# Optimization experiments

Measured on AMD Instinct MI355X. Metric: run time of the kernel, lower is better.

Reference implementation:

```python
import jax, jax.numpy as jnp
import numpy as np

B, S, DIM, HEADS, DH = 1, 192, 512, 8, 64
LN_EPS = 1e-5


def setup_inputs() -> dict:
    key = jax.random.key(0)
    ks = jax.random.split(key, 5)
    rn = lambda k, shp: jax.random.normal(k, shp, dtype=jnp.float32) * 0.02
    return {
        "x": jax.random.normal(ks[0], (B, S, DIM), dtype=jnp.float32),
        "ln_w": jnp.ones((DIM,), jnp.float32),
        "ln_b": jnp.zeros((DIM,), jnp.float32),
        "W_abcde": rn(ks[1], (5 * HEADS * DH, DIM)),
        "b_abcde": jnp.zeros((5 * HEADS * DH,), jnp.float32),
        "W_K": rn(ks[2], (HEADS, DH, DH, DH)),
        "W_V": rn(ks[3], (HEADS, DH, DH, DH)),
        "W_out": rn(ks[4], (DIM, HEADS * DH)),
        "b_out": jnp.zeros((DIM,), jnp.float32),
    }


def reference(x, ln_w, ln_b, W_abcde, b_abcde, W_K, W_V, W_out, b_out):
    b, n, _ = x.shape
    # LayerNorm (biased variance, eps=1e-5, affine)
    mu = jnp.mean(x, axis=-1, keepdims=True)
    var = jnp.var(x, axis=-1, keepdims=True)
    xn = (x - mu) / jnp.sqrt(var + LN_EPS) * ln_w + ln_b
    # abcde projection, chunk into 5, split heads -> [b, n, h, d]
    proj = xn @ W_abcde.T + b_abcde
    a_, b_, c_, d_, e_ = [t.reshape(b, n, HEADS, DH) for t in jnp.split(proj, 5, axis=-1)]
    # cubic attention score chain (note: heads summed out in step2, reintroduced by a_)
    step1 = jnp.einsum('brnk,nijk->brij', c_, W_K)          # [b, r, d, d]
    step2 = jnp.einsum('brij,bqnj->briq', step1, b_)        # [b, r, d, q] (sum over heads of b_)
    attn = jnp.einsum('briq,bpni->bnpqr', step2, a_)        # [b, h, p, q, r]
    # "causal" mask: positions where p >= q set to 1e-6 (faithful to masked_fill_)
    t_idx = jnp.arange(n)[:, None, None]
    s_idx = jnp.arange(n)[None, :, None]
    mask = (t_idx >= s_idx)[None, None]                      # [1,1,p,q,1]
    attn = jnp.where(mask, jnp.float32(1e-6), attn)
    # 'b n p1 p2 p3 -> b n p3 (p1 p2)', scale by 1/dim_head, softmax over (p1 p2)
    attn = attn.transpose(0, 1, 4, 2, 3).reshape(b, HEADS, n, n * n) / DH
    attn = jax.nn.softmax(attn, axis=-1)
    # pairwise values: [b, p1, p2, h, d] -> 'b p s n h -> b n h (p s)'
    v = jnp.einsum('bpnh,bqng,nhgf->bpqnf', d_, e_, W_V)
    v = v.transpose(0, 3, 4, 1, 2).reshape(b, HEADS, DH, n * n)
    # weighted sum over pair axis, merge heads
    z = jnp.einsum('bnql,bnhl->bqnh', attn, v).reshape(b, n, HEADS * DH)
    return z @ W_out.T + b_out
```

## Files before the change

### kernel.cpp

```cpp
#include <hip/hip_runtime.h>
#include <hip/hip_bf16.h>
#include <cstdint>

#define SEQ 192

typedef float f32x4 __attribute__((ext_vector_type(4)));
typedef float f32x8 __attribute__((ext_vector_type(8)));
typedef __bf16 bf16;
typedef __bf16 bf16x8 __attribute__((ext_vector_type(8)));
typedef __bf16 bf16x4 __attribute__((ext_vector_type(4)));

#define MFMA_BF16(a, b, c) __builtin_amdgcn_mfma_f32_16x16x32_bf16(a, b, c, 0, 0, 0)

__device__ __forceinline__ bf16x8 cvt8(f32x8 v) {
  bf16x8 o;
#pragma unroll
  for (int i = 0; i < 8; i++) o[i] = (bf16)v[i];
  return o;
}

__global__ __launch_bounds__(256) void k1_prep(
    const float* __restrict__ x, const float* __restrict__ ln_w, const float* __restrict__ ln_b,
    const float* __restrict__ WV, bf16* __restrict__ xn_bf, bf16* __restrict__ WVt2) {
  int bid = blockIdx.x, tid = threadIdx.x;
  if (bid < 512) {
    int g = bid & 63, hh = bid >> 6;
    __shared__ float ld[64 * 65];
    int f = tid & 63, r4 = tid >> 6;
#pragma unroll
    for (int it = 0; it < 16; it++) {
      int hp = it * 4 + r4;
      ld[hp * 65 + f] = WV[(((size_t)(hh * 64 + hp) * 64 + g) * 64) + f];
    }
    __syncthreads();
    int hp2 = tid & 63;
#pragma unroll
    for (int it = 0; it < 16; it++) {
      int ff = it * 4 + r4;
      WVt2[(size_t)hh * 262144 + (size_t)(ff * 64 + g) * 64 + hp2] = (bf16)ld[hp2 * 65 + ff];
    }
    return;
  }
  bid -= 512;
  {
    int r = bid;
    const float* xr = x + (size_t)r * 512;
    float v0 = xr[tid], v1 = xr[tid + 256];
    float s = v0 + v1, s2 = v0 * v0 + v1 * v1;
#pragma unroll
    for (int off = 32; off > 0; off >>= 1) {
      s += __shfl_down(s, off);
      s2 += __shfl_down(s2, off);
    }
    __shared__ float redS[4], redS2[4];
    int wave = tid >> 6, lane = tid & 63;
    if (lane == 0) { redS[wave] = s; redS2[wave] = s2; }
    __syncthreads();
    float S = redS[0] + redS[1] + redS[2] + redS[3];
    float S2 = redS2[0] + redS2[1] + redS2[2] + redS2[3];
    float mean = S * (1.0f / 512.0f);
    float var = S2 * (1.0f / 512.0f) - mean * mean;
    float rstd = rsqrtf(var + 1e-5f);
    bf16* xnr = xn_bf + (size_t)r * 512;
    xnr[tid] = (bf16)((v0 - mean) * rstd * ln_w[tid] + ln_b[tid]);
    xnr[tid + 256] = (bf16)((v1 - mean) * rstd * ln_w[tid + 256] + ln_b[tid + 256]);
  }
}

template <int MODE>
__device__ __forceinline__ void gemm_body(const bf16* __restrict__ A, const bf16* __restrict__ Bt,
                                          bf16* __restrict__ C1, int N, int K,
                                          int nb, int mb, int tid) {
  int n0 = nb * 64, m0 = mb * 64;
  int wave = tid >> 6, lane = tid & 63;
  int lq = lane >> 4, l16 = lane & 15;
  const bf16* Ap = A + (size_t)(m0 + wave * 16 + l16) * K;
  f32x4 acc[4];
#pragma unroll
  for (int nt = 0; nt < 4; nt++) acc[nt] = (f32x4){0.f, 0.f, 0.f, 0.f};
  for (int k0 = 0; k0 < K; k0 += 32) {
    bf16x8 af = *(const bf16x8*)(Ap + k0 + lq * 8);
#pragma unroll
    for (int nt = 0; nt < 4; nt++) {
      bf16x8 bv = *(const bf16x8*)(Bt + (size_t)(n0 + nt * 16 + l16) * K + k0 + lq * 8);
      acc[nt] = MFMA_BF16(af, bv, acc[nt]);
    }
  }
  int cm = m0 + wave * 16 + lq * 4;
#pragma unroll
  for (int nt = 0; nt < 4; nt++) {
    int n = n0 + nt * 16 + l16;
    if constexpr (MODE == 1) {
#pragma unroll
      for (int rg = 0; rg < 4; rg++) C1[(size_t)(cm + rg) * N + n] = (bf16)acc[nt][rg];
    } else {
      int r = cm >> 6, i0 = cm & 63;
      bf16x4 pk = {(bf16)acc[nt][0], (bf16)acc[nt][1], (bf16)acc[nt][2], (bf16)acc[nt][3]};
      *(bf16x4*)(C1 + (size_t)r * 12288 + (size_t)n * 64 + i0) = pk;
    }
  }
}

__global__ __launch_bounds__(256) void k2_proj(
    const bf16* __restrict__ xn_bf, const float* __restrict__ Wab,
    const float* __restrict__ b_abcde, float* __restrict__ proj, bf16* __restrict__ a_bf,
    bf16* __restrict__ c_bf, bf16* __restrict__ d_bf) {
  int bid = blockIdx.x, tid = threadIdx.x;
  int nb = bid % 40, mb = bid / 40;
  int n0 = nb * 64, m0 = mb * 64;
  int wave = tid >> 6, lane = tid & 63;
  int lq = lane >> 4, l16 = lane & 15;
  const bf16* Ap = xn_bf + (size_t)(m0 + wave * 16 + l16) * 512;
  f32x4 acc[4];
#pragma unroll
  for (int nt = 0; nt < 4; nt++) acc[nt] = (f32x4){0.f, 0.f, 0.f, 0.f};
  for (int k0 = 0; k0 < 512; k0 += 32) {
    bf16x8 af = *(const bf16x8*)(Ap + k0 + lq * 8);
#pragma unroll
    for (int nt = 0; nt < 4; nt++) {
      f32x8 wv = *(const f32x8*)(Wab + (size_t)(n0 + nt * 16 + l16) * 512 + k0 + lq * 8);
      acc[nt] = MFMA_BF16(af, cvt8(wv), acc[nt]);
    }
  }
  int cm = m0 + wave * 16 + lq * 4;
#pragma unroll
  for (int nt = 0; nt < 4; nt++) {
    int n = n0 + nt * 16 + l16;
    int chunk = n >> 9, hcol = (n >> 6) & 7, i = n & 63;
#pragma unroll
    for (int rg = 0; rg < 4; rg++) {
      int m = cm + rg;
      float v = acc[nt][rg] + b_abcde[n];
      proj[(size_t)m * 2560 + n] = v;
      bf16 bv = (bf16)v;
      if (chunk == 0) a_bf[((size_t)hcol * SEQ + m) * 64 + i] = bv;
      else if (chunk == 2) c_bf[(size_t)m * 512 + (n - 1024)] = bv;
      else if (chunk == 3) d_bf[((size_t)hcol * SEQ + m) * 64 + i] = bv;
    }
  }
}

__global__ __launch_bounds__(256) void k3_mid(
    const bf16* __restrict__ c_bf, const float* __restrict__ WK, bf16* __restrict__ s1bf,
    const bf16* __restrict__ d_bf, const bf16* __restrict__ WVt2, bf16* __restrict__ tTt,
    const float* __restrict__ proj, bf16* __restrict__ eT_bf, float* __restrict__ ecum,
    bf16* __restrict__ bsum_bf) {
  __shared__ float el[64 * 65];
  int bid = blockIdx.x, tid = threadIdx.x;
  if (bid < 192) {
    int nb = bid % 64, mb = bid / 64;
    int n0 = nb * 64, m0 = mb * 64;
    int wave = tid >> 6, lane = tid & 63;
    int lq = lane >> 4, l16 = lane & 15;
    const bf16* Ap = c_bf + (size_t)(m0 + wave * 16 + l16) * 512;
    f32x4 acc[4];
#pragma unroll
    for (int nt = 0; nt < 4; nt++) acc[nt] = (f32x4){0.f, 0.f, 0.f, 0.f};
    size_t offn[4];
#pragma unroll
    for (int nt = 0; nt < 4; nt++) {
      int n = n0 + nt * 16 + l16;
      offn[nt] = (size_t)(n >> 6) * 4096 + (size_t)(n & 63) * 64;
    }
    for (int k0 = 0; k0 < 512; k0 += 32) {
      bf16x8 af = *(const bf16x8*)(Ap + k0 + lq * 8);
      size_t kb = (size_t)(k0 >> 6) * 262144 + (k0 & 32) + lq * 8;
#pragma unroll
      for (int nt = 0; nt < 4; nt++) {
        f32x8 wv = *(const f32x8*)(WK + kb + offn[nt]);
        acc[nt] = MFMA_BF16(af, cvt8(wv), acc[nt]);
      }
    }
    int cm = m0 + wave * 16 + lq * 4;
#pragma unroll
    for (int nt = 0; nt < 4; nt++) {
      int n = n0 + nt * 16 + l16;
#pragma unroll
      for (int rg = 0; rg < 4; rg++) s1bf[(size_t)(cm + rg) * 4096 + n] = (bf16)acc[nt][rg];
    }
    return;
  }
  bid -= 192;
  if (bid < 1536) {
    int h = bid / 192, rem = bid % 192;
    gemm_body<1>(d_bf + (size_t)h * 12288, WVt2 + (size_t)h * 262144,
                 tTt + (size_t)h * 786432, 4096, 64, rem % 64, rem / 64, tid);
    return;
  }
  bid -= 1536;
  if (bid < 8) {
    int h = bid;
    float carry = 0.f;
    for (int ch = 0; ch < 3; ch++) {
      int pbase = ch * 64;
      for (int idx = tid; idx < 4096; idx += 256) {
        int pl = idx >> 6, g = idx & 63;
        el[pl * 65 + g] = proj[(size_t)(pbase + pl) * 2560 + 2048 + h * 64 + g];
      }
      __syncthreads();
      for (int idx = tid; idx < 4096; idx += 256) {
        int g = idx >> 6, ql = idx & 63;
        eT_bf[((size_t)h * 64 + g) * SEQ + pbase + ql] = (bf16)el[ql * 65 + g];
      }
      if (tid < 64) {
        float run = carry;
        for (int pl = 0; pl < 64; pl++) {
          run += el[pl * 65 + tid];
          ecum[(size_t)h * 12288 + (pbase + pl) * 64 + tid] = run;
        }
        carry = run;
      }
      __syncthreads();
    }
    return;
  }
  bid -= 8;
  {
    int j = tid & 63, qg = tid >> 6;
#pragma unroll
    for (int qi = 0; qi < 16; qi++) {
      int q = bid * 64 + qg * 16 + qi;
      float s = 0.f;
#pragma unroll
      for (int hh = 0; hh < 8; hh++) s += proj[(size_t)q * 2560 + 512 + hh * 64 + j];
      bsum_bf[q * 64 + j] = (bf16)s;
    }
  }
}

__global__ __launch_bounds__(256) void k4_step2(const bf16* __restrict__ s1bf,
                                                const bf16* __restrict__ bsum_bf,
                                                bf16* __restrict__ s2bf) {
  int bid = blockIdx.x;
  gemm_body<2>(s1bf, bsum_bf, s2bf, 192, 64, bid % 3, bid / 3, threadIdx.x);
}

__global__ __launch_bounds__(256, 3) void k5_attn(
    const bf16* __restrict__ a_bf, const bf16* __restrict__ s2bf,
    const bf16* __restrict__ eT_bf, const float* __restrict__ ecum,
    bf16* __restrict__ ew_bf, float* __restrict__ Lsum) {
  int r = blockIdx.x, h = blockIdx.y;
  int tid = threadIdx.x, wave = tid >> 6, lane = tid & 63;
  int lq = lane >> 4, l16 = lane & 15;
  __shared__ __align__(16) bf16 wch[2][4][3][16 * 40];
  __shared__ float redL[4];
  int pt[3] = {wave, wave + 4, 11 - wave};

  const bf16* ah = a_bf + (size_t)h * 12288;
  const bf16* s2r = s2bf + (size_t)r * 12288;
  const bf16* eh = eT_bf + (size_t)h * 12288;
  const float* ech = ecum + (size_t)h * 12288;

  bf16x8 afr[3][2];
#pragma unroll
  for (int mt = 0; mt < 3; mt++)
#pragma unroll
    for (int kc = 0; kc < 2; kc++)
      afr[mt][kc] = *(const bf16x8*)(ah + (pt[mt] * 16 + l16) * 64 + kc * 32 + lq * 8);

  f32x4 ewacc[3][4];
#pragma unroll
  for (int mt = 0; mt < 3; mt++)
#pragma unroll
    for (int nt = 0; nt < 4; nt++) ewacc[mt][nt] = (f32x4){0.f, 0.f, 0.f, 0.f};
  float lpart = 0.f;

  for (int c = 0; c < 6; c++) {
    if (c * 32 + 31 <= wave * 16) continue;
    int par = c & 1;
    bf16x8 efr[4];
#pragma unroll
    for (int nt = 0; nt < 4; nt++)
      efr[nt] = *(const bf16x8*)(eh + (nt * 16 + l16) * SEQ + c * 32 + lq * 8);
    bf16x8 bq[2][2];
#pragma unroll
    for (int sub = 0; sub < 2; sub++) {
      int q = c * 32 + sub * 16 + l16;
      bq[sub][0] = *(const bf16x8*)(s2r + q * 64 + lq * 8);
      bq[sub][1] = *(const bf16x8*)(s2r + q * 64 + 32 + lq * 8);
    }
    f32x4 sacc[3][2];
#pragma unroll
    for (int mt = 0; mt < 3; mt++) {
      if (c * 32 + 31 <= pt[mt] * 16) continue;
#pragma unroll
      for (int sub = 0; sub < 2; sub++) {
        if (c * 32 + sub * 16 + 15 <= pt[mt] * 16) continue;
        f32x4 sv = (f32x4){0.f, 0.f, 0.f, 0.f};
        sv = MFMA_BF16(afr[mt][0], bq[sub][0], sv);
        sacc[mt][sub] = MFMA_BF16(afr[mt][1], bq[sub][1], sv);
      }
    }
#pragma unroll
    for (int mt = 0; mt < 3; mt++) {
      if (c * 32 + 31 <= pt[mt] * 16) continue;
      bf16* mybuf = &wch[par][wave][mt][0];
#pragma unroll
      for (int sub = 0; sub < 2; sub++) {
        if (c * 32 + sub * 16 + 15 <= pt[mt] * 16) {
#pragma unroll
          for (int rg = 0; rg < 4; rg++) mybuf[(lq * 4 + rg) * 40 + sub * 16 + l16] = (bf16)0.f;
          continue;
        }
        int q = c * 32 + sub * 16 + l16;
        int p0 = pt[mt] * 16 + lq * 4;
#pragma unroll
        for (int rg = 0; rg < 4; rg++) {
          float wv = (q > p0 + rg) ? __expf(sacc[mt][sub][rg] * 0.015625f) : 0.f;
          lpart += wv;
          mybuf[(lq * 4 + rg) * 40 + sub * 16 + l16] = (bf16)wv;
        }
      }
    }
#pragma unroll
    for (int mt = 0; mt < 3; mt++) {
      if (c * 32 + 31 <= pt[mt] * 16) continue;
      bf16x8 wf = *(const bf16x8*)(&wch[par][wave][mt][l16 * 40 + lq * 8]);
#pragma unroll
      for (int nt = 0; nt < 4; nt++) ewacc[mt][nt] = MFMA_BF16(wf, efr[nt], ewacc[mt][nt]);
    }
  }

  bf16* ewout = ew_bf + ((size_t)h * SEQ + r) * 12288;
#pragma unroll
  for (int mt = 0; mt < 3; mt++)
#pragma unroll
    for (int nt = 0; nt < 4; nt++)
#pragma unroll
      for (int rg = 0; rg < 4; rg++) {
        int p = pt[mt] * 16 + lq * 4 + rg;
        int g = nt * 16 + l16;
        ewout[p * 64 + g] = (bf16)(ewacc[mt][nt][rg] + ech[p * 64 + g]);
      }

#pragma unroll
  for (int off = 32; off > 0; off >>= 1) lpart += __shfl_down(lpart, off);
  if (lane == 0) redL[wave] = lpart;
  __syncthreads();
  if (tid == 0) Lsum[h * SEQ + r] = redL[0] + redL[1] + redL[2] + redL[3];
}

__global__ __launch_bounds__(512) void k5b_z(
    const bf16* __restrict__ ew_bf, const bf16* __restrict__ tTt, float* __restrict__ Zpart) {
  int h = blockIdx.x, mt = blockIdx.y, ks = blockIdx.z;
  int tid = threadIdx.x, wave = tid >> 6, lane = tid & 63;
  int lq = lane >> 4, l16 = lane & 15;
  __shared__ float zred[8][16][66];
  const bf16* ewh = ew_bf + ((size_t)h * SEQ + mt * 32) * 12288;
  const bf16* th = tTt + (size_t)h * 786432;
  f32x4 acc[2][4];
#pragma unroll
  for (int m2 = 0; m2 < 2; m2++)
#pragma unroll
    for (int nt = 0; nt < 4; nt++) acc[m2][nt] = (f32x4){0.f, 0.f, 0.f, 0.f};
  for (int jj = 0; jj < 6; jj++) {
    int kc = ks * 48 + wave * 6 + jj;
    int p = kc >> 1, g0 = (kc & 1) * 32;
    bf16x8 af0 = *(const bf16x8*)(ewh + (size_t)l16 * 12288 + kc * 32 + lq * 8);
    bf16x8 af1 = *(const bf16x8*)(ewh + (size_t)(16 + l16) * 12288 + kc * 32 + lq * 8);
#pragma unroll
    for (int nt = 0; nt < 4; nt++) {
      bf16x8 tf = *(const bf16x8*)(th + (size_t)p * 4096 + (nt * 16 + l16) * 64 + g0 + lq * 8);
      acc[0][nt] = MFMA_BF16(af0, tf, acc[0][nt]);
      acc[1][nt] = MFMA_BF16(af1, tf, acc[1][nt]);
    }
  }
#pragma unroll
  for (int m2 = 0; m2 < 2; m2++) {
    if (m2) __syncthreads();
#pragma unroll
    for (int nt = 0; nt < 4; nt++)
#pragma unroll
      for (int rg = 0; rg < 4; rg++) zred[wave][lq * 4 + rg][nt * 16 + l16] = acc[m2][nt][rg];
    __syncthreads();
#pragma unroll
    for (int o = 0; o < 2; o++) {
      int idx = o * 512 + tid;
      int rloc = idx >> 6, f = idx & 63;
      float s = 0.f;
#pragma unroll
      for (int wv = 0; wv < 8; wv++) s += zred[wv][rloc][f];
      Zpart[(size_t)ks * 98304 + (size_t)(mt * 32 + m2 * 16 + rloc) * 512 + h * 64 + f] = s;
    }
  }
}

__global__ __launch_bounds__(256) void k5c_zf(const float* __restrict__ Zpart,
                                              const float* __restrict__ Lsum,
                                              bf16* __restrict__ z_bf) {
  int m = blockIdx.x, tid = threadIdx.x;
#pragma unroll
  for (int o = 0; o < 2; o++) {
    int c = o * 256 + tid;
    int h = c >> 6;
    float s = 0.f;
#pragma unroll
    for (int ks = 0; ks < 8; ks++) s += Zpart[(size_t)ks * 98304 + (size_t)m * 512 + c];
    float L = Lsum[h * SEQ + m] + 18528.0f;
    z_bf[(size_t)m * 512 + c] = (bf16)(s / L);
  }
}

__global__ __launch_bounds__(256) void k6_out(
    const bf16* __restrict__ z_bf, const float* __restrict__ Wout,
    const float* __restrict__ b_out, float* __restrict__ out) {
  int bid = blockIdx.x, tid = threadIdx.x;
  int nb = bid & 7, mb = bid >> 3;
  int wave = tid >> 6, lane = tid & 63;
  int lq = lane >> 4, l16 = lane & 15;
  int m = mb * 16 + l16;
  f32x4 acc[4];
#pragma unroll
  for (int nt = 0; nt < 4; nt++) acc[nt] = (f32x4){0.f, 0.f, 0.f, 0.f};
#pragma unroll
  for (int kc = 0; kc < 4; kc++) {
    int k0 = wave * 128 + kc * 32;
    bf16x8 af = *(const bf16x8*)(z_bf + (size_t)m * 512 + k0 + lq * 8);
#pragma unroll
    for (int nt = 0; nt < 4; nt++) {
      f32x8 wv = *(const f32x8*)(Wout + (size_t)(nb * 64 + nt * 16 + l16) * 512 + k0 + lq * 8);
      acc[nt] = MFMA_BF16(af, cvt8(wv), acc[nt]);
    }
  }
  __shared__ float red[4][16][68];
#pragma unroll
  for (int nt = 0; nt < 4; nt++)
#pragma unroll
    for (int rg = 0; rg < 4; rg++) red[wave][lq * 4 + rg][nt * 16 + l16] = acc[nt][rg];
  __syncthreads();
#pragma unroll
  for (int o = 0; o < 4; o++) {
    int idx = o * 256 + tid;
    int rloc = idx >> 6, f = idx & 63;
    float s = red[0][rloc][f] + red[1][rloc][f] + red[2][rloc][f] + red[3][rloc][f];
    out[(size_t)(mb * 16 + rloc) * 512 + nb * 64 + f] = s + b_out[nb * 64 + f];
  }
}

static const size_t OFF_PROJ = 0;
static const size_t OFF_ECUM = 491520;
static const size_t OFF_XN = 589824;
static const size_t OFF_ZPART = 638976;
static const size_t OFF_LSUM = 1425408;
static const size_t OFF_Z = 1427456;
static const size_t OFF_WVT = 2473984;
static const size_t OFF_A = 3522560;
static const size_t OFF_C = 3571712;
static const size_t OFF_D = 3620864;
static const size_t OFF_ET = 3670016;
static const size_t OFF_BSUM = 3719168;
static const size_t OFF_S1 = 3725312;
static const size_t OFF_S2 = 4118528;
static const size_t OFF_TT = 5298176;
static const size_t OFF_EW = 8493056;

extern "C" void kernel_launch(void* const* d_in, const int* in_sizes, int n_in,
                              void* d_out, int out_size, void* d_ws, size_t ws_size,
                              hipStream_t stream) {
  (void)in_sizes; (void)n_in; (void)out_size; (void)ws_size;
  const float* x = (const float*)d_in[0];
  const float* ln_w = (const float*)d_in[1];
  const float* ln_b = (const float*)d_in[2];
  const float* W_abcde = (const float*)d_in[3];
  const float* b_abcde = (const float*)d_in[4];
  const float* W_K = (const float*)d_in[5];
  const float* W_V = (const float*)d_in[6];
  const float* W_out = (const float*)d_in[7];
  const float* b_out = (const float*)d_in[8];
  float* out = (float*)d_out;
  float* ws = (float*)d_ws;

  float* proj = ws + OFF_PROJ;
  float* ecum = ws + OFF_ECUM;
  bf16* xn_bf = (bf16*)(ws + OFF_XN);
  float* Zpart = ws + OFF_ZPART;
  float* Lsum = ws + OFF_LSUM;
  bf16* z_bf = (bf16*)(ws + OFF_Z);
  bf16* WVt2 = (bf16*)(ws + OFF_WVT);
  bf16* a_bf = (bf16*)(ws + OFF_A);
  bf16* c_bf = (bf16*)(ws + OFF_C);
  bf16* d_bf = (bf16*)(ws + OFF_D);
  bf16* eT_bf = (bf16*)(ws + OFF_ET);
  bf16* bsum_bf = (bf16*)(ws + OFF_BSUM);
  bf16* s1bf = (bf16*)(ws + OFF_S1);
  bf16* s2bf = (bf16*)(ws + OFF_S2);
  bf16* tTt = (bf16*)(ws + OFF_TT);
  bf16* ew_bf = (bf16*)(ws + OFF_EW);

  k1_prep<<<704, 256, 0, stream>>>(x, ln_w, ln_b, W_V, xn_bf, WVt2);
  k2_proj<<<120, 256, 0, stream>>>(xn_bf, W_abcde, b_abcde, proj, a_bf, c_bf, d_bf);
  k3_mid<<<1739, 256, 0, stream>>>(c_bf, W_K, s1bf, d_bf, WVt2, tTt, proj, eT_bf, ecum,
                                   bsum_bf);
  k4_step2<<<576, 256, 0, stream>>>(s1bf, bsum_bf, s2bf);
  k5_attn<<<dim3(SEQ, 8), 256, 0, stream>>>(a_bf, s2bf, eT_bf, ecum, ew_bf, Lsum);
  k5b_z<<<dim3(8, 6, 8), 512, 0, stream>>>(ew_bf, tTt, Zpart);
  k5c_zf<<<SEQ, 256, 0, stream>>>(Zpart, Lsum, z_bf);
  k6_out<<<96, 256, 0, stream>>>(z_bf, W_out, b_out, out);
}
```

Before: 214.9 us.

## Fuse pipeline into one cooperative persistent kernel with grid syncs

Measured after the change: 588.3 us. +173.8%, slower.

```diff
diff --git a/kernel.cpp b/kernel.cpp
--- a/kernel.cpp
+++ b/kernel.cpp
@@ -1,8 +1,12 @@
 #include <hip/hip_runtime.h>
+#include <hip/hip_cooperative_groups.h>
 #include <hip/hip_bf16.h>
 #include <cstdint>
 
+namespace cg = cooperative_groups;
+
 #define SEQ 192
+#define GRID 512
 
 typedef float f32x4 __attribute__((ext_vector_type(4)));
 typedef float f32x8 __attribute__((ext_vector_type(8)));
@@ -19,32 +23,67 @@
   return o;
 }
 
-__global__ __launch_bounds__(256) void k1_prep(
-    const float* __restrict__ x, const float* __restrict__ ln_w, const float* __restrict__ ln_b,
-    const float* __restrict__ WV, bf16* __restrict__ xn_bf, bf16* __restrict__ WVt2) {
-  int bid = blockIdx.x, tid = threadIdx.x;
-  if (bid < 512) {
-    int g = bid & 63, hh = bid >> 6;
-    __shared__ float ld[64 * 65];
+struct P {
+  const float *x, *ln_w, *ln_b, *Wab, *b_ab, *WK, *WV, *Wout, *b_out;
+  float *out, *proj, *ecum, *Zpart, *Lsum;
+  bf16 *xn, *WVt2, *a, *c, *d, *eT, *bsum, *s1, *s2, *tTt, *ew;
+};
+
+template <int MODE>
+__device__ __forceinline__ void gemm_body(const bf16* __restrict__ A, const bf16* __restrict__ Bt,
+                                          bf16* __restrict__ C1, int N, int K, int nb, int mb,
+                                          int tid) {
+  int n0 = nb * 64, m0 = mb * 64;
+  int wave = tid >> 6, lane = tid & 63;
+  int lq = lane >> 4, l16 = lane & 15;
+  const bf16* Ap = A + (size_t)(m0 + wave * 16 + l16) * K;
+  f32x4 acc[4];
+#pragma unroll
+  for (int nt = 0; nt < 4; nt++) acc[nt] = (f32x4){0.f, 0.f, 0.f, 0.f};
+  for (int k0 = 0; k0 < K; k0 += 32) {
+    bf16x8 af = *(const bf16x8*)(Ap + k0 + lq * 8);
+#pragma unroll
+    for (int nt = 0; nt < 4; nt++) {
+      bf16x8 bv = *(const bf16x8*)(Bt + (size_t)(n0 + nt * 16 + l16) * K + k0 + lq * 8);
+      acc[nt] = MFMA_BF16(af, bv, acc[nt]);
+    }
+  }
+  int cm = m0 + wave * 16 + lq * 4;
+#pragma unroll
+  for (int nt = 0; nt < 4; nt++) {
+    int n = n0 + nt * 16 + l16;
+    if constexpr (MODE == 1) {
+#pragma unroll
+      for (int rg = 0; rg < 4; rg++) C1[(size_t)(cm + rg) * N + n] = (bf16)acc[nt][rg];
+    } else {
+      int r = cm >> 6, i0 = cm & 63;
+      bf16x4 pk = {(bf16)acc[nt][0], (bf16)acc[nt][1], (bf16)acc[nt][2], (bf16)acc[nt][3]};
+      *(bf16x4*)(C1 + (size_t)r * 12288 + (size_t)n * 64 + i0) = pk;
+    }
+  }
+}
+
+__device__ __forceinline__ void ph1(const P& p, char* sm, int u, int tid) {
+  if (u < 512) {
+    int g = u & 63, hh = u >> 6;
+    float* ld = (float*)sm;
     int f = tid & 63, r4 = tid >> 6;
 #pragma unroll
     for (int it = 0; it < 16; it++) {
       int hp = it * 4 + r4;
-      ld[hp * 65 + f] = WV[(((size_t)(hh * 64 + hp) * 64 + g) * 64) + f];
+      ld[hp * 65 + f] = p.WV[(((size_t)(hh * 64 + hp) * 64 + g) * 64) + f];
     }
     __syncthreads();
     int hp2 = tid & 63;
 #pragma unroll
     for (int it = 0; it < 16; it++) {
       int ff = it * 4 + r4;
-      WVt2[(size_t)hh * 262144 + (size_t)(ff * 64 + g) * 64 + hp2] = (bf16)ld[hp2 * 65 + ff];
-    }
-    return;
-  }
-  bid -= 512;
-  {
-    int r = bid;
-    const float* xr = x + (size_t)r * 512;
+      p.WVt2[(size_t)hh * 262144 + (size_t)(ff * 64 + g) * 64 + hp2] = (bf16)ld[hp2 * 65 + ff];
+    }
+    __syncthreads();
+  } else {
+    int r = u - 512;
+    const float* xr = p.x + (size_t)r * 512;
     float v0 = xr[tid], v1 = xr[tid + 256];
     float s = v0 + v1, s2 = v0 * v0 + v1 * v1;
 #pragma unroll
@@ -52,7 +91,8 @@
       s += __shfl_down(s, off);
       s2 += __shfl_down(s2, off);
     }
-    __shared__ float redS[4], redS2[4];
+    float* redS = (float*)(sm + 16640);
+    float* redS2 = redS + 4;
     int wave = tid >> 6, lane = tid & 63;
     if (lane == 0) { redS[wave] = s; redS2[wave] = s2; }
     __syncthreads();
@@ -61,56 +101,19 @@
     float mean = S * (1.0f / 512.0f);
     float var = S2 * (1.0f / 512.0f) - mean * mean;
     float rstd = rsqrtf(var + 1e-5f);
-    bf16* xnr = xn_bf + (size_t)r * 512;
-    xnr[tid] = (bf16)((v0 - mean) * rstd * ln_w[tid] + ln_b[tid]);
-    xnr[tid + 256] = (bf16)((v1 - mean) * rstd * ln_w[tid + 256] + ln_b[tid + 256]);
-  }
-}
-
-template <int MODE>
-__device__ __forceinline__ void gemm_body(const bf16* __restrict__ A, const bf16* __restrict__ Bt,
-                                          bf16* __restrict__ C1, int N, int K,
-                                          int nb, int mb, int tid) {
+    bf16* xnr = p.xn + (size_t)r * 512;
+    xnr[tid] = (bf16)((v0 - mean) * rstd * p.ln_w[tid] + p.ln_b[tid]);
+    xnr[tid + 256] = (bf16)((v1 - mean) * rstd * p.ln_w[tid + 256] + p.ln_b[tid + 256]);
+    __syncthreads();
+  }
+}
+
+__device__ __forceinline__ void ph2(const P& p, int u, int tid) {
+  int nb = u % 40, mb = u / 40;
   int n0 = nb * 64, m0 = mb * 64;
   int wave = tid >> 6, lane = tid & 63;
   int lq = lane >> 4, l16 = lane & 15;
-  const bf16* Ap = A + (size_t)(m0 + wave * 16 + l16) * K;
-  f32x4 acc[4];
-#pragma unroll
-  for (int nt = 0; nt < 4; nt++) acc[nt] = (f32x4){0.f, 0.f, 0.f, 0.f};
-  for (int k0 = 0; k0 < K; k0 += 32) {
-    bf16x8 af = *(const bf16x8*)(Ap + k0 + lq * 8);
-#pragma unroll
-    for (int nt = 0; nt < 4; nt++) {
-      bf16x8 bv = *(const bf16x8*)(Bt + (size_t)(n0 + nt * 16 + l16) * K + k0 + lq * 8);
-      acc[nt] = MFMA_BF16(af, bv, acc[nt]);
-    }
-  }
-  int cm = m0 + wave * 16 + lq * 4;
-#pragma unroll
-  for (int nt = 0; nt < 4; nt++) {
-    int n = n0 + nt * 16 + l16;
-    if constexpr (MODE == 1) {
-#pragma unroll
-      for (int rg = 0; rg < 4; rg++) C1[(size_t)(cm + rg) * N + n] = (bf16)acc[nt][rg];
-    } else {
-      int r = cm >> 6, i0 = cm & 63;
-      bf16x4 pk = {(bf16)acc[nt][0], (bf16)acc[nt][1], (bf16)acc[nt][2], (bf16)acc[nt][3]};
-      *(bf16x4*)(C1 + (size_t)r * 12288 + (size_t)n * 64 + i0) = pk;
-    }
-  }
-}
-
-__global__ __launch_bounds__(256) void k2_proj(
-    const bf16* __restrict__ xn_bf, const float* __restrict__ Wab,
-    const float* __restrict__ b_abcde, float* __restrict__ proj, bf16* __restrict__ a_bf,
-    bf16* __restrict__ c_bf, bf16* __restrict__ d_bf) {
-  int bid = blockIdx.x, tid = threadIdx.x;
-  int nb = bid % 40, mb = bid / 40;
-  int n0 = nb * 64, m0 = mb * 64;
-  int wave = tid >> 6, lane = tid & 63;
-  int lq = lane >> 4, l16 = lane & 15;
-  const bf16* Ap = xn_bf + (size_t)(m0 + wave * 16 + l16) * 512;
+  const bf16* Ap = p.xn + (size_t)(m0 + wave * 16 + l16) * 512;
   f32x4 acc[4];
 #pragma unroll
   for (int nt = 0; nt < 4; nt++) acc[nt] = (f32x4){0.f, 0.f, 0.f, 0.f};
@@ -118,7 +121,7 @@
     bf16x8 af = *(const bf16x8*)(Ap + k0 + lq * 8);
 #pragma unroll
     for (int nt = 0; nt < 4; nt++) {
-      f32x8 wv = *(const f32x8*)(Wab + (size_t)(n0 + nt * 16 + l16) * 512 + k0 + lq * 8);
+      f32x8 wv = *(const f32x8*)(p.Wab + (size_t)(n0 + nt * 16 + l16) * 512 + k0 + lq * 8);
       acc[nt] = MFMA_BF16(af, cvt8(wv), acc[nt]);
     }
   }
@@ -130,126 +133,106 @@
 #pragma unroll
     for (int rg = 0; rg < 4; rg++) {
       int m = cm + rg;
-      float v = acc[nt][rg] + b_abcde[n];
-      proj[(size_t)m * 2560 + n] = v;
+      float v = acc[nt][rg] + p.b_ab[n];
+      p.proj[(size_t)m * 2560 + n] = v;
       bf16 bv = (bf16)v;
-      if (chunk == 0) a_bf[((size_t)hcol * SEQ + m) * 64 + i] = bv;
-      else if (chunk == 2) c_bf[(size_t)m * 512 + (n - 1024)] = bv;
-      else if (chunk == 3) d_bf[((size_t)hcol * SEQ + m) * 64 + i] = bv;
-    }
-  }
-}
-
-__global__ __launch_bounds__(256) void k3_mid(
-    const bf16* __restrict__ c_bf, const float* __restrict__ WK, bf16* __restrict__ s1bf,
-    const bf16* __restrict__ d_bf, const bf16* __restrict__ WVt2, bf16* __restrict__ tTt,
-    const float* __restrict__ proj, bf16* __restrict__ eT_bf, float* __restrict__ ecum,
-    bf16* __restrict__ bsum_bf) {
-  __shared__ float el[64 * 65];
-  int bid = blockIdx.x, tid = threadIdx.x;
-  if (bid < 192) {
-    int nb = bid % 64, mb = bid / 64;
-    int n0 = nb * 64, m0 = mb * 64;
-    int wave = tid >> 6, lane = tid & 63;
-    int lq = lane >> 4, l16 = lane & 15;
-    const bf16* Ap = c_bf + (size_t)(m0 + wave * 16 + l16) * 512;
-    f32x4 acc[4];
-#pragma unroll
-    for (int nt = 0; nt < 4; nt++) acc[nt] = (f32x4){0.f, 0.f, 0.f, 0.f};
-    size_t offn[4];
-#pragma unroll
-    for (int nt = 0; nt < 4; nt++) {
-      int n = n0 + nt * 16 + l16;
-      offn[nt] = (size_t)(n >> 6) * 4096 + (size_t)(n & 63) * 64;
-    }
-    for (int k0 = 0; k0 < 512; k0 += 32) {
-      bf16x8 af = *(const bf16x8*)(Ap + k0 + lq * 8);
-      size_t kb = (size_t)(k0 >> 6) * 262144 + (k0 & 32) + lq * 8;
-#pragma unroll
-      for (int nt = 0; nt < 4; nt++) {
-        f32x8 wv = *(const f32x8*)(WK + kb + offn[nt]);
-        acc[nt] = MFMA_BF16(af, cvt8(wv), acc[nt]);
-      }
-    }
-    int cm = m0 + wave * 16 + lq * 4;
-#pragma unroll
-    for (int nt = 0; nt < 4; nt++) {
-      int n = n0 + nt * 16 + l16;
-#pragma unroll
-      for (int rg = 0; rg < 4; rg++) s1bf[(size_t)(cm + rg) * 4096 + n] = (bf16)acc[nt][rg];
-    }
-    return;
-  }
-  bid -= 192;
-  if (bid < 1536) {
-    int h = bid / 192, rem = bid % 192;
-    gemm_body<1>(d_bf + (size_t)h * 12288, WVt2 + (size_t)h * 262144,
-                 tTt + (size_t)h * 786432, 4096, 64, rem % 64, rem / 64, tid);
-    return;
-  }
-  bid -= 1536;
-  if (bid < 8) {
-    int h = bid;
+      if (chunk == 0) p.a[((size_t)hcol * SEQ + m) * 64 + i] = bv;
+      else if (chunk == 2) p.c[(size_t)m * 512 + (n - 1024)] = bv;
+      else if (chunk == 3) p.d[((size_t)hcol * SEQ + m) * 64 + i] = bv;
+    }
+  }
+}
+
+__device__ __forceinline__ void ph3(const P& p, char* sm, int u, int tid) {
+  if (u < 8) {
+    int h = u;
+    float* el = (float*)sm;
     float carry = 0.f;
     for (int ch = 0; ch < 3; ch++) {
       int pbase = ch * 64;
+      if (ch) __syncthreads();
       for (int idx = tid; idx < 4096; idx += 256) {
         int pl = idx >> 6, g = idx & 63;
-        el[pl * 65 + g] = proj[(size_t)(pbase + pl) * 2560 + 2048 + h * 64 + g];
+        el[pl * 65 + g] = p.proj[(size_t)(pbase + pl) * 2560 + 2048 + h * 64 + g];
       }
       __syncthreads();
       for (int idx = tid; idx < 4096; idx += 256) {
         int g = idx >> 6, ql = idx & 63;
-        eT_bf[((size_t)h * 64 + g) * SEQ + pbase + ql] = (bf16)el[ql * 65 + g];
+        p.eT[((size_t)h * 64 + g) * SEQ + pbase + ql] = (bf16)el[ql * 65 + g];
       }
       if (tid < 64) {
         float run = carry;
         for (int pl = 0; pl < 64; pl++) {
           run += el[pl * 65 + tid];
-          ecum[(size_t)h * 12288 + (pbase + pl) * 64 + tid] = run;
+          p.ecum[(size_t)h * 12288 + (pbase + pl) * 64 + tid] = run;
         }
         carry = run;
       }
       __syncthreads();
     }
-    return;
-  }
-  bid -= 8;
-  {
+  } else if (u < 11) {
+    int b3 = u - 8;
     int j = tid & 63, qg = tid >> 6;
 #pragma unroll
     for (int qi = 0; qi < 16; qi++) {
-      int q = bid * 64 + qg * 16 + qi;
+      int q = b3 * 64 + qg * 16 + qi;
       float s = 0.f;
 #pragma unroll
-      for (int hh = 0; hh < 8; hh++) s += proj[(size_t)q * 2560 + 512 + hh * 64 + j];
-      bsum_bf[q * 64 + j] = (bf16)s;
-    }
-  }
-}
-
-__global__ __launch_bounds__(256) void k4_step2(const bf16* __restrict__ s1bf,
-                                                const bf16* __restrict__ bsum_bf,
-                                                bf16* __restrict__ s2bf) {
-  int bid = blockIdx.x;
-  gemm_body<2>(s1bf, bsum_bf, s2bf, 192, 64, bid % 3, bid / 3, threadIdx.x);
-}
-
-__global__ __launch_bounds__(256, 3) void k5_attn(
-    const bf16* __restrict__ a_bf, const bf16* __restrict__ s2bf,
-    const bf16* __restrict__ eT_bf, const float* __restrict__ ecum,
-    bf16* __restrict__ ew_bf, float* __restrict__ Lsum) {
-  int r = blockIdx.x, h = blockIdx.y;
-  int tid = threadIdx.x, wave = tid >> 6, lane = tid & 63;
+      for (int hh = 0; hh < 8; hh++) s += p.proj[(size_t)q * 2560 + 512 + hh * 64 + j];
+      p.bsum[q * 64 + j] = (bf16)s;
+    }
+  } else if (u < 203) {
+    int unit = u - 11;
+    int nb = unit & 63, mb = unit >> 6;
+    int n0 = nb * 64, m0 = mb * 64;
+    int wave = tid >> 6, lane = tid & 63;
+    int lq = lane >> 4, l16 = lane & 15;
+    const bf16* Ap = p.c + (size_t)(m0 + wave * 16 + l16) * 512;
+    f32x4 acc[4];
+#pragma unroll
+    for (int nt = 0; nt < 4; nt++) acc[nt] = (f32x4){0.f, 0.f, 0.f, 0.f};
+    size_t offn[4];
+#pragma unroll
+    for (int nt = 0; nt < 4; nt++) {
+      int n = n0 + nt * 16 + l16;
+      offn[nt] = (size_t)(n >> 6) * 4096 + (size_t)(n & 63) * 64;
+    }
+    for (int k0 = 0; k0 < 512; k0 += 32) {
+      bf16x8 af = *(const bf16x8*)(Ap + k0 + lq * 8);
+      size_t kb = (size_t)(k0 >> 6) * 262144 + (k0 & 32) + lq * 8;
+#pragma unroll
+      for (int nt = 0; nt < 4; nt++) {
+        f32x8 wv = *(const f32x8*)(p.WK + kb + offn[nt]);
+        acc[nt] = MFMA_BF16(af, cvt8(wv), acc[nt]);
+      }
+    }
+    int cm = m0 + wave * 16 + lq * 4;
+#pragma unroll
+    for (int nt = 0; nt < 4; nt++) {
+      int n = n0 + nt * 16 + l16;
+#pragma unroll
+      for (int rg = 0; rg < 4; rg++) p.s1[(size_t)(cm + rg) * 4096 + n] = (bf16)acc[nt][rg];
+    }
+  } else {
+    int unit = u - 203;
+    int h = unit / 192, rem = unit % 192;
+    gemm_body<1>(p.d + (size_t)h * 12288, p.WVt2 + (size_t)h * 262144,
+                 p.tTt + (size_t)h * 786432, 4096, 64, rem % 64, rem / 64, tid);
+  }
+}
+
+__device__ __forceinline__ void ph5(const P& p, char* sm, int u, int tid) {
+  int h = u & 7, r = u >> 3;
+  int wave = tid >> 6, lane = tid & 63;
   int lq = lane >> 4, l16 = lane & 15;
-  __shared__ __align__(16) bf16 wch[2][4][3][16 * 40];
-  __shared__ float redL[4];
+  bf16* wch = (bf16*)sm;
+  float* redL = (float*)(sm + 30720);
   int pt[3] = {wave, wave + 4, 11 - wave};
 
-  const bf16* ah = a_bf + (size_t)h * 12288;
-  const bf16* s2r = s2bf + (size_t)r * 12288;
-  const bf16* eh = eT_bf + (size_t)h * 12288;
-  const float* ech = ecum + (size_t)h * 12288;
+  const bf16* ah = p.a + (size_t)h * 12288;
+  const bf16* s2r = p.s2 + (size_t)r * 12288;
+  const bf16* eh = p.eT + (size_t)h * 12288;
+  const float* ech = p.ecum + (size_t)h * 12288;
 
   bf16x8 afr[3][2];
 #pragma unroll
@@ -265,27 +248,27 @@
     for (int nt = 0; nt < 4; nt++) ewacc[mt][nt] = (f32x4){0.f, 0.f, 0.f, 0.f};
   float lpart = 0.f;
 
-  for (int c = 0; c < 6; c++) {
-    if (c * 32 + 31 <= wave * 16) continue;
-    int par = c & 1;
+  for (int cc = 0; cc < 6; cc++) {
+    if (cc * 32 + 31 <= wave * 16) continue;
+    int par = cc & 1;
     bf16x8 efr[4];
 #pragma unroll
     for (int nt = 0; nt < 4; nt++)
-      efr[nt] = *(const bf16x8*)(eh + (nt * 16 + l16) * SEQ + c * 32 + lq * 8);
+      efr[nt] = *(const bf16x8*)(eh + (nt * 16 + l16) * SEQ + cc * 32 + lq * 8);
     bf16x8 bq[2][2];
 #pragma unroll
     for (int sub = 0; sub < 2; sub++) {
-      int q = c * 32 + sub * 16 + l16;
+      int q = cc * 32 + sub * 16 + l16;
       bq[sub][0] = *(const bf16x8*)(s2r + q * 64 + lq * 8);
       bq[sub][1] = *(const bf16x8*)(s2r + q * 64 + 32 + lq * 8);
     }
     f32x4 sacc[3][2];
 #pragma unroll
     for (int mt = 0; mt < 3; mt++) {
-      if (c * 32 + 31 <= pt[mt] * 16) continue;
+      if (cc * 32 + 31 <= pt[mt] * 16) continue;
 #pragma unroll
       for (int sub = 0; sub < 2; sub++) {
-        if (c * 32 + sub * 16 + 15 <= pt[mt] * 16) continue;
+        if (cc * 32 + sub * 16 + 15 <= pt[mt] * 16) continue;
         f32x4 sv = (f32x4){0.f, 0.f, 0.f, 0.f};
         sv = MFMA_BF16(afr[mt][0], bq[sub][0], sv);
         sacc[mt][sub] = MFMA_BF16(afr[mt][1], bq[sub][1], sv);
@@ -293,16 +276,16 @@
     }
 #pragma unroll
     for (int mt = 0; mt < 3; mt++) {
-      if (c * 32 + 31 <= pt[mt] * 16) continue;
-      bf16* mybuf = &wch[par][wave][mt][0];
+      if (cc * 32 + 31 <= pt[mt] * 16) continue;
+      bf16* mybuf = wch + ((par * 4 + wave) * 3 + mt) * 640;
 #pragma unroll
       for (int sub = 0; sub < 2; sub++) {
-        if (c * 32 + sub * 16 + 15 <= pt[mt] * 16) {
+        if (cc * 32 + sub * 16 + 15 <= pt[mt] * 16) {
 #pragma unroll
           for (int rg = 0; rg < 4; rg++) mybuf[(lq * 4 + rg) * 40 + sub * 16 + l16] = (bf16)0.f;
           continue;
         }
-        int q = c * 32 + sub * 16 + l16;
+        int q = cc * 32 + sub * 16 + l16;
         int p0 = pt[mt] * 16 + lq * 4;
 #pragma unroll
         for (int rg = 0; rg < 4; rg++) {
@@ -314,53 +297,54 @@
     }
 #pragma unroll
     for (int mt = 0; mt < 3; mt++) {
-      if (c * 32 + 31 <= pt[mt] * 16) continue;
-      bf16x8 wf = *(const bf16x8*)(&wch[par][wave][mt][l16 * 40 + lq * 8]);
+      if (cc * 32 + 31 <= pt[mt] * 16) continue;
+      bf16x8 wf = *(const bf16x8*)(wch + ((par * 4 + wave) * 3 + mt) * 640 + l16 * 40 + lq * 8);
 #pragma unroll
       for (int nt = 0; nt < 4; nt++) ewacc[mt][nt] = MFMA_BF16(wf, efr[nt], ewacc[mt][nt]);
     }
   }
 
-  bf16* ewout = ew_bf + ((size_t)h * SEQ + r) * 12288;
+  bf16* ewout = p.ew + ((size_t)h * SEQ + r) * 12288;
 #pragma unroll
   for (int mt = 0; mt < 3; mt++)
 #pragma unroll
     for (int nt = 0; nt < 4; nt++)
 #pragma unroll
       for (int rg = 0; rg < 4; rg++) {
-        int p = pt[mt] * 16 + lq * 4 + rg;
+        int pp = pt[mt] * 16 + lq * 4 + rg;
         int g = nt * 16 + l16;
-        ewout[p * 64 + g] = (bf16)(ewacc[mt][nt][rg] + ech[p * 64 + g]);
+        ewout[pp * 64 + g] = (bf16)(ewacc[mt][nt][rg] + ech[pp * 64 + g]);
       }
 
 #pragma unroll
   for (int off = 32; off > 0; off >>= 1) lpart += __shfl_down(lpart, off);
   if (lane == 0) redL[wave] = lpart;
   __syncthreads();
-  if (tid == 0) Lsum[h * SEQ + r] = redL[0] + redL[1] + redL[2] + redL[3];
-}
-
-__global__ __launch_bounds__(512) void k5b_z(
-    const bf16* __restrict__ ew_bf, const bf16* __restrict__ tTt, float* __restrict__ Zpart) {
-  int h = blockIdx.x, mt = blockIdx.y, ks = blockIdx.z;
-  int tid = threadIdx.x, wave = tid >> 6, lane = tid & 63;
+  if (tid == 0) p.Lsum[h * SEQ + r] = redL[0] + redL[1] + redL[2] + redL[3];
+  __syncthreads();
+}
+
+__device__ __forceinline__ void ph6(const P& p, char* sm, int u, int tid) {
+  int ks = u & 15, mtb = (u >> 4) % 6, h = u / 96;
+  int wave = tid >> 6, lane = tid & 63;
   int lq = lane >> 4, l16 = lane & 15;
-  __shared__ float zred[8][16][66];
-  const bf16* ewh = ew_bf + ((size_t)h * SEQ + mt * 32) * 12288;
-  const bf16* th = tTt + (size_t)h * 786432;
+  float* zred = (float*)sm;
+  const bf16* ewh = p.ew + ((size_t)h * SEQ + mtb * 32) * 12288;
+  const bf16* th = p.tTt + (size_t)h * 786432;
   f32x4 acc[2][4];
 #pragma unroll
   for (int m2 = 0; m2 < 2; m2++)
 #pragma unroll
     for (int nt = 0; nt < 4; nt++) acc[m2][nt] = (f32x4){0.f, 0.f, 0.f, 0.f};
+#pragma unroll
   for (int jj = 0; jj < 6; jj++) {
-    int kc = ks * 48 + wave * 6 + jj;
-    int p = kc >> 1, g0 = (kc & 1) * 32;
+    int kc = ks * 24 + wave * 6 + jj;
+    int pp = kc >> 1, g0 = (kc & 1) * 32;
     bf16x8 af0 = *(const bf16x8*)(ewh + (size_t)l16 * 12288 + kc * 32 + lq * 8);
     bf16x8 af1 = *(const bf16x8*)(ewh + (size_t)(16 + l16) * 12288 + kc * 32 + lq * 8);
 #pragma unroll
     for (int nt = 0; nt < 4; nt++) {
-      bf16x8 tf = *(const bf16x8*)(th + (size_t)p * 4096 + (nt * 16 + l16) * 64 + g0 + lq * 8);
+      bf16x8 tf = *(const bf16x8*)(th + (size_t)pp * 4096 + (nt * 16 + l16) * 64 + g0 + lq * 8);
       acc[0][nt] = MFMA_BF16(af0, tf, acc[0][nt]);
       acc[1][nt] = MFMA_BF16(af1, tf, acc[1][nt]);
     }
@@ -371,129 +355,172 @@
 #pragma unroll
     for (int nt = 0; nt < 4; nt++)
 #pragma unroll
-      for (int rg = 0; rg < 4; rg++) zred[wave][lq * 4 + rg][nt * 16 + l16] = acc[m2][nt][rg];
+      for (int rg = 0; rg < 4; rg++)
+        zred[(wave * 16 + lq * 4 + rg) * 66 + nt * 16 + l16] = acc[m2][nt][rg];
     __syncthreads();
 #pragma unroll
-    for (int o = 0; o < 2; o++) {
-      int idx = o * 512 + tid;
+    for (int o = 0; o < 4; o++) {
+      int idx = o * 256 + tid;
       int rloc = idx >> 6, f = idx & 63;
-      float s = 0.f;
-#pragma unroll
-      for (int wv = 0; wv < 8; wv++) s += zred[wv][rloc][f];
-      Zpart[(size_t)ks * 98304 + (size_t)(mt * 32 + m2 * 16 + rloc) * 512 + h * 64 + f] = s;
-    }
-  }
-}
-
-__global__ __launch_bounds__(256) void k5c_zf(const float* __restrict__ Zpart,
-                                              const float* __restrict__ Lsum,
-                                              bf16* __restrict__ z_bf) {
-  int m = blockIdx.x, tid = threadIdx.x;
-#pragma unroll
-  for (int o = 0; o < 2; o++) {
-    int c = o * 256 + tid;
-    int h = c >> 6;
+      float s = zred[rloc * 66 + f] + zred[(16 + rloc) * 66 + f] + zred[(32 + rloc) * 66 + f] +
+                zred[(48 + rloc) * 66 + f];
+      p.Zpart[(size_t)ks * 98304 + (size_t)(mtb * 32 + m2 * 16 + rloc) * 512 + h * 64 + f] = s;
+    }
+  }
+  __syncthreads();
+}
+
+__device__ __forceinline__ void ph7(const P& p, char* sm, int u, int tid) {
+  int mb = u >> 3, nb = u & 7;
+  bf16* zt = (bf16*)sm;
+  float* rd = (float*)(sm + 16640);
+  for (int idx = tid; idx < 8192; idx += 256) {
+    int m = idx >> 9, cc = idx & 511;
     float s = 0.f;
 #pragma unroll
-    for (int ks = 0; ks < 8; ks++) s += Zpart[(size_t)ks * 98304 + (size_t)m * 512 + c];
-    float L = Lsum[h * SEQ + m] + 18528.0f;
-    z_bf[(size_t)m * 512 + c] = (bf16)(s / L);
-  }
-}
-
-__global__ __launch_bounds__(256) void k6_out(
-    const bf16* __restrict__ z_bf, const float* __restrict__ Wout,
-    const float* __restrict__ b_out, float* __restrict__ out) {
-  int bid = blockIdx.x, tid = threadIdx.x;
-  int nb = bid & 7, mb = bid >> 3;
+    for (int ks = 0; ks < 16; ks++)
+      s += p.Zpart[(size_t)ks * 98304 + (size_t)(mb * 16 + m) * 512 + cc];
+    float L = p.Lsum[(cc >> 6) * SEQ + mb * 16 + m] + 18528.0f;
+    zt[m * 520 + cc] = (bf16)(s / L);
+  }
+  __syncthreads();
   int wave = tid >> 6, lane = tid & 63;
   int lq = lane >> 4, l16 = lane & 15;
-  int m = mb * 16 + l16;
   f32x4 acc[4];
 #pragma unroll
   for (int nt = 0; nt < 4; nt++) acc[nt] = (f32x4){0.f, 0.f, 0.f, 0.f};
 #pragma unroll
   for (int kc = 0; kc < 4; kc++) {
     int k0 = wave * 128 + kc * 32;
-    bf16x8 af = *(const bf16x8*)(z_bf + (size_t)m * 512 + k0 + lq * 8);
+    bf16x8 af = *(const bf16x8*)(zt + l16 * 520 + k0 + lq * 8);
 #pragma unroll
     for (int nt = 0; nt < 4; nt++) {
-      f32x8 wv = *(const f32x8*)(Wout + (size_t)(nb * 64 + nt * 16 + l16) * 512 + k0 + lq * 8);
+      f32x8 wv = *(const f32x8*)(p.Wout + (size_t)(nb * 64 + nt * 16 + l16) * 512 + k0 + lq * 8);
       acc[nt] = MFMA_BF16(af, cvt8(wv), acc[nt]);
     }
   }
-  __shared__ float red[4][16][68];
+  __syncthreads();
 #pragma unroll
   for (int nt = 0; nt < 4; nt++)
 #pragma unroll
-    for (int rg = 0; rg < 4; rg++) red[wave][lq * 4 + rg][nt * 16 + l16] = acc[nt][rg];
+    for (int rg = 0; rg < 4; rg++)
+      rd[(wave * 16 + lq * 4 + rg) * 68 + nt * 16 + l16] = acc[nt][rg];
   __syncthreads();
 #pragma unroll
   for (int o = 0; o < 4; o++) {
     int idx = o * 256 + tid;
     int rloc = idx >> 6, f = idx & 63;
-    float s = red[0][rloc][f] + red[1][rloc][f] + red[2][rloc][f] + red[3][rloc][f];
-    out[(size_t)(mb * 16 + rloc) * 512 + nb * 64 + f] = s + b_out[nb * 64 + f];
-  }
+    float s = rd[rloc * 68 + f] + rd[(16 + rloc) * 68 + f] + rd[(32 + rloc) * 68 + f] +
+              rd[(48 + rloc) * 68 + f];
+    p.out[(size_t)(mb * 16 + rloc) * 512 + nb * 64 + f] = s + p.b_out[nb * 64 + f];
+  }
+}
+
+__global__ __launch_bounds__(256, 2) void mega(P p) {
+  cg::grid_group grid = cg::this_grid();
+  __shared__ __align__(16) char sm[34816];
+  int tid = threadIdx.x;
+  for (int u = blockIdx.x; u < 704; u += GRID) ph1(p, sm, u, tid);
+  grid.sync();
+  for (int u = blockIdx.x; u < 120; u += GRID) ph2(p, u, tid);
+  grid.sync();
+  for (int u = blockIdx.x; u < 1739; u += GRID) ph3(p, sm, u, tid);
+  grid.sync();
+  for (int u = blockIdx.x; u < 576; u += GRID)
+    gemm_body<2>(p.s1, p.bsum, p.s2, 192, 64, u % 3, u / 3, tid);
+  grid.sync();
+  for (int u = blockIdx.x; u < 1536; u += GRID) ph5(p, sm, u, tid);
+  grid.sync();
+  for (int u = blockIdx.x; u < 768; u += GRID) ph6(p, sm, u, tid);
+  grid.sync();
+  for (int u = blockIdx.x; u < 96; u += GRID) ph7(p, sm, u, tid);
+}
+
+__global__ __launch_bounds__(256) void g1(P p) {
+  __shared__ __align__(16) char sm[16672];
+  ph1(p, sm, blockIdx.x, threadIdx.x);
+}
+__global__ __launch_bounds__(256) void g2(P p) { ph2(p, blockIdx.x, threadIdx.x); }
+__global__ __launch_bounds__(256) void g3(P p) {
+  __shared__ __align__(16) char sm[16640];
+  ph3(p, sm, blockIdx.x, threadIdx.x);
+}
+__global__ __launch_bounds__(256) void g4(P p) {
+  int u = blockIdx.x;
+  gemm_body<2>(p.s1, p.bsum, p.s2, 192, 64, u % 3, u / 3, threadIdx.x);
+}
+__global__ __launch_bounds__(256, 3) void g5(P p) {
+  __shared__ __align__(16) char sm[30736];
+  ph5(p, sm, blockIdx.x, threadIdx.x);
+}
+__global__ __launch_bounds__(256) void g6(P p) {
+  __shared__ __align__(16) char sm[16896];
+  ph6(p, sm, blockIdx.x, threadIdx.x);
+}
+__global__ __launch_bounds__(256) void g7(P p) {
+  __shared__ __align__(16) char sm[34048];
+  ph7(p, sm, blockIdx.x, threadIdx.x);
 }
 
 static const size_t OFF_PROJ = 0;
 static const size_t OFF_ECUM = 491520;
 static const size_t OFF_XN = 589824;
-static const size_t OFF_ZPART = 638976;
-static const size_t OFF_LSUM = 1425408;
-static const size_t OFF_Z = 1427456;
-static const size_t OFF_WVT = 2473984;
-static const size_t OFF_A = 3522560;
-static const size_t OFF_C = 3571712;
-static const size_t OFF_D = 3620864;
-static const size_t OFF_ET = 3670016;
-static const size_t OFF_BSUM = 3719168;
-static const size_t OFF_S1 = 3725312;
-static const size_t OFF_S2 = 4118528;
-static const size_t OFF_TT = 5298176;
-static const size_t OFF_EW = 8493056;
+static const size_t OFF_LSUM = 638976;
+static const size_t OFF_ZPART = 640512;
+static const size_t OFF_WVT = 2213376;
+static const size_t OFF_A = 3261952;
+static const size_t OFF_C = 3311104;
+static const size_t OFF_D = 3360256;
+static const size_t OFF_ET = 3409408;
+static const size_t OFF_BSUM = 3458560;
+static const size_t OFF_S1 = 3464704;
+static const size_t OFF_S2 = 3857920;
+static const size_t OFF_TT = 5037568;
+static const size_t OFF_EW = 8183296;
 
 extern "C" void kernel_launch(void* const* d_in, const int* in_sizes, int n_in,
                               void* d_out, int out_size, void* d_ws, size_t ws_size,
                               hipStream_t stream) {
   (void)in_sizes; (void)n_in; (void)out_size; (void)ws_size;
-  const float* x = (const float*)d_in[0];
-  const float* ln_w = (const float*)d_in[1];
-  const float* ln_b = (const float*)d_in[2];
-  const float* W_abcde = (const float*)d_in[3];
-  const float* b_abcde = (const float*)d_in[4];
-  const float* W_K = (const float*)d_in[5];
-  const float* W_V = (const float*)d_in[6];
-  const float* W_out = (const float*)d_in[7];
-  const float* b_out = (const float*)d_in[8];
-  float* out = (float*)d_out;
   float* ws = (float*)d_ws;
-
-  float* proj = ws + OFF_PROJ;
-  float* ecum = ws + OFF_ECUM;
-  bf16* xn_bf = (bf16*)(ws + OFF_XN);
-  float* Zpart = ws + OFF_ZPART;
-  float* Lsum = ws + OFF_LSUM;
-  bf16* z_bf = (bf16*)(ws + OFF_Z);
-  bf16* WVt2 = (bf16*)(ws + OFF_WVT);
-  bf16* a_bf = (bf16*)(ws + OFF_A);
-  bf16* c_bf = (bf16*)(ws + OFF_C);
-  bf16* d_bf = (bf16*)(ws + OFF_D);
-  bf16* eT_bf = (bf16*)(ws + OFF_ET);
-  bf16* bsum_bf = (bf16*)(ws + OFF_BSUM);
-  bf16* s1bf = (bf16*)(ws + OFF_S1);
-  bf16* s2bf = (bf16*)(ws + OFF_S2);
-  bf16* tTt = (bf16*)(ws + OFF_TT);
-  bf16* ew_bf = (bf16*)(ws + OFF_EW);
-
-  k1_prep<<<704, 256, 0, stream>>>(x, ln_w, ln_b, W_V, xn_bf, WVt2);
-  k2_proj<<<120, 256, 0, stream>>>(xn_bf, W_abcde, b_abcde, proj, a_bf, c_bf, d_bf);
-  k3_mid<<<1739, 256, 0, stream>>>(c_bf, W_K, s1bf, d_bf, WVt2, tTt, proj, eT_bf, ecum,
-                                   bsum_bf);
-  k4_step2<<<576, 256, 0, stream>>>(s1bf, bsum_bf, s2bf);
-  k5_attn<<<dim3(SEQ, 8), 256, 0, stream>>>(a_bf, s2bf, eT_bf, ecum, ew_bf, Lsum);
-  k5b_z<<<dim3(8, 6, 8), 512, 0, stream>>>(ew_bf, tTt, Zpart);
-  k5c_zf<<<SEQ, 256, 0, stream>>>(Zpart, Lsum, z_bf);
-  k6_out<<<96, 256, 0, stream>>>(z_bf, W_out, b_out, out);
-}
+  P p;
+  p.x = (const float*)d_in[0];
+  p.ln_w = (const float*)d_in[1];
+  p.ln_b = (const float*)d_in[2];
+  p.Wab = (const float*)d_in[3];
+  p.b_ab = (const float*)d_in[4];
+  p.WK = (const float*)d_in[5];
+  p.WV = (const float*)d_in[6];
+  p.Wout = (const float*)d_in[7];
+  p.b_out = (const float*)d_in[8];
+  p.out = (float*)d_out;
+  p.proj = ws + OFF_PROJ;
+  p.ecum = ws + OFF_ECUM;
+  p.Zpart = ws + OFF_ZPART;
+  p.Lsum = ws + OFF_LSUM;
+  p.xn = (bf16*)(ws + OFF_XN);
+  p.WVt2 = (bf16*)(ws + OFF_WVT);
+  p.a = (bf16*)(ws + OFF_A);
+  p.c = (bf16*)(ws + OFF_C);
+  p.d = (bf16*)(ws + OFF_D);
+  p.eT = (bf16*)(ws + OFF_ET);
+  p.bsum = (bf16*)(ws + OFF_BSUM);
+  p.s1 = (bf16*)(ws + OFF_S1);
+  p.s2 = (bf16*)(ws + OFF_S2);
+  p.tTt = (bf16*)(ws + OFF_TT);
+  p.ew = (bf16*)(ws + OFF_EW);
+
+  void* args[] = {(void*)&p};
+  hipError_t err = hipLaunchCooperativeKernel((const void*)mega, dim3(GRID), dim3(256), args,
+                                              0, stream);
+  if (err != hipSuccess) {
+    (void)hipGetLastError();
+    g1<<<704, 256, 0, stream>>>(p);
+    g2<<<120, 256, 0, stream>>>(p);
+    g3<<<1739, 256, 0, stream>>>(p);
+    g4<<<576, 256, 0, stream>>>(p);
+    g5<<<1536, 256, 0, stream>>>(p);
+    g6<<<768, 256, 0, stream>>>(p);
+    g7<<<96, 256, 0, stream>>>(p);
+  }
+}
```
